# Performance work log

Hardware: AMD Instinct MI355X
Metric: run time of the kernel (lower is better)

Reference implementation:

```python
import jax, jax.numpy as jnp
import numpy as np

H = 16  # num_heads

def setup_inputs() -> dict:
    key = jax.random.key(0)
    ks = jax.random.split(key, 6)
    B, N, D = 2, 2048, 1024
    s = 0.02
    return {
        "x": jax.random.normal(ks[0], (B, N, D), jnp.float32),
        "attn_bias": jax.random.normal(ks[1], (B, N), jnp.float32),
        "w_qkv": jax.random.normal(ks[2], (D, 3 * D), jnp.float32) * s,
        "b_qkv": jnp.zeros((3 * D,), jnp.float32),
        "w_proj": jax.random.normal(ks[3], (D, D), jnp.float32) * s,
        "b_proj": jnp.zeros((D,), jnp.float32),
    }

def reference(x, attn_bias, w_qkv, b_qkv, w_proj, b_proj):
    B, N, D = x.shape
    hd = D // H
    qkv = x @ w_qkv + b_qkv                       # (B,N,3D)
    qkv = qkv.reshape(B, N, 3, H, hd)
    q, k, v = qkv[:, :, 0], qkv[:, :, 1], qkv[:, :, 2]  # (B,N,H,hd)
    scores = jnp.einsum("bqhd,bkhd->bhqk", q, k) / np.sqrt(hd).astype(x.dtype)
    scores = scores + attn_bias[:, None, None, :]  # key-wise bias (B,1,1,N)
    w = jax.nn.softmax(scores, axis=-1)
    out = jnp.einsum("bhqk,bkhd->bqhd", w, v).reshape(B, N, D)
    return out @ w_proj + b_proj
```

## Files before the change

kernel.cpp:

```cpp
#include <hip/hip_runtime.h>
#include <stdint.h>

typedef __attribute__((ext_vector_type(8))) short bf16x8;
typedef __attribute__((ext_vector_type(4))) short s16x4;
typedef __attribute__((ext_vector_type(4))) float f32x4;
typedef __attribute__((ext_vector_type(2))) unsigned int u32x2;
typedef __attribute__((ext_vector_type(4))) unsigned int u32x4;

#define DEV __device__ __forceinline__

DEV unsigned short f2bf(float f) {
    unsigned u = __builtin_bit_cast(unsigned, f);
    u += 0x7FFFu + ((u >> 16) & 1u);
    return (unsigned short)(u >> 16);
}

DEV void gload_lds16(const void* g, void* l) {
    __builtin_amdgcn_global_load_lds(
        (const __attribute__((address_space(1))) unsigned int*)g,
        (__attribute__((address_space(3))) unsigned int*)l,
        16, 0, 0);
}

__global__ __launch_bounds__(256) void cvt_f32_bf16(
    const float* __restrict__ in, unsigned short* __restrict__ out, int n4) {
    int i = blockIdx.x * blockDim.x + threadIdx.x;
    if (i >= n4) return;
    const float4 v = reinterpret_cast<const float4*>(in)[i];
    s16x4 o;
    o.x = (short)f2bf(v.x); o.y = (short)f2bf(v.y);
    o.z = (short)f2bf(v.z); o.w = (short)f2bf(v.w);
    reinterpret_cast<s16x4*>(out)[i] = o;
}

__global__ __launch_bounds__(256) void transpose_w(
    const float* __restrict__ w, unsigned short* __restrict__ wt, int K, int N) {
    __shared__ unsigned short tile[64][72];
    const int k0 = blockIdx.y * 64, n0 = blockIdx.x * 64;
    const int t = threadIdx.x;
    #pragma unroll
    for (int i = 0; i < 4; ++i) {
        const int e = t + i * 256;
        const int r = e >> 4, c4 = e & 15;
        const float4 v = *reinterpret_cast<const float4*>(w + (size_t)(k0 + r) * N + n0 + c4 * 4);
        s16x4 o;
        o.x = (short)f2bf(v.x); o.y = (short)f2bf(v.y);
        o.z = (short)f2bf(v.z); o.w = (short)f2bf(v.w);
        *(s16x4*)&tile[r][c4 * 4] = o;
    }
    __syncthreads();
    #pragma unroll
    for (int i = 0; i < 4; ++i) {
        const int e = t + i * 256;
        const int rn = e >> 4, c4 = e & 15;
        s16x4 o;
        o.x = (short)tile[c4 * 4 + 0][rn];
        o.y = (short)tile[c4 * 4 + 1][rn];
        o.z = (short)tile[c4 * 4 + 2][rn];
        o.w = (short)tile[c4 * 4 + 3][rn];
        *(s16x4*)(wt + (size_t)(n0 + rn) * K + k0 + c4 * 4) = o;
    }
}

__global__ __launch_bounds__(512, 2)
void gemm256_qkv(const unsigned short* __restrict__ A,
                 const unsigned short* __restrict__ BT,
                 const float* __restrict__ bias,
                 unsigned short* __restrict__ q_out,
                 unsigned short* __restrict__ k_out,
                 unsigned short* __restrict__ v_out)
{
    constexpr int K = 1024;
    constexpr int NT = 16;
    __shared__ unsigned short lds[2][2][2][2][128][32];

    const int t = threadIdx.x;
    const int wave = t >> 6, lane = t & 63;
    const int l15 = lane & 15, l4 = lane >> 4;
    const int wr = wave >> 2, wc = wave & 3;

    const int lin = blockIdx.x;
    const int logical = (lin & 7) * 24 + (lin >> 3);
    const int bx = logical % 12, by = logical / 12;
    const int tile_m = by * 256, tile_n = bx * 256;

    const int st_row = t >> 2;
    const int st_col = ((t & 3) ^ ((t >> 3) & 3)) * 8;
    const int cswz   = (l4 ^ ((l15 >> 1) & 3)) * 8;

    f32x4 acc[8][4] = {};
    bf16x8 ra[4], rb[4];

    #define STAGE(buf, ab, half, kk, k0)                                           \
        gload_lds16(((ab) ? BT : A) +                                              \
                        (size_t)(((ab) ? tile_n : tile_m) + (half) * 128 + st_row) * K \
                        + (k0) + (kk) * 32 + st_col,                               \
                    &lds[buf][ab][half][kk][0][0] + wave * 512)
    #define READ_A(buf, kk, mq)                                                    \
        _Pragma("unroll") for (int i = 0; i < 4; ++i)                              \
            ra[i] = *(const bf16x8*)&lds[buf][0][wr][kk][((mq) * 4 + i) * 16 + l15][cswz];
    #define READ_B(buf, kk)                                                        \
        _Pragma("unroll") for (int n = 0; n < 4; ++n)                              \
            rb[n] = *(const bf16x8*)&lds[buf][1][wc >> 1][kk][(wc & 1) * 64 + n * 16 + l15][cswz];
    #define MFMA16(mq)                                                             \
        __builtin_amdgcn_s_setprio(1);                                             \
        _Pragma("unroll") for (int i = 0; i < 4; ++i)                              \
            _Pragma("unroll") for (int n = 0; n < 4; ++n)                          \
                acc[(mq) * 4 + i][n] = __builtin_amdgcn_mfma_f32_16x16x32_bf16(    \
                    ra[i], rb[n], acc[(mq) * 4 + i][n], 0, 0, 0);                  \
        __builtin_amdgcn_s_setprio(0);
    #define BAR()   __builtin_amdgcn_s_barrier()
    #define LGKM0() do { asm volatile("s_waitcnt lgkmcnt(0)" ::: "memory");        \
                         __builtin_amdgcn_sched_barrier(0); } while (0)

    STAGE(0, 1, 0, 0, 0);  STAGE(0, 1, 1, 0, 0);
    STAGE(0, 0, 0, 0, 0);  STAGE(0, 0, 1, 0, 0);
    STAGE(0, 1, 0, 1, 0);  STAGE(0, 1, 1, 1, 0);
    STAGE(0, 0, 0, 1, 0);  STAGE(0, 0, 1, 1, 0);
    STAGE(1, 1, 0, 0, 64); STAGE(1, 1, 1, 0, 64);
    STAGE(1, 0, 0, 0, 64); STAGE(1, 0, 1, 0, 64);
    STAGE(1, 1, 0, 1, 64); STAGE(1, 1, 1, 1, 64);
    asm volatile("s_waitcnt vmcnt(6)" ::: "memory");
    BAR();

    for (int kt = 0; kt < NT; ++kt) {
        const int buf = kt & 1;
        const int k0 = kt * 64;
        const bool s1 = (kt + 1 < NT);
        const bool s234 = (kt + 2 < NT);

        READ_A(buf, 0, 0); READ_B(buf, 0);
        if (s1) { STAGE(buf ^ 1, 0, 0, 1, k0 + 64); STAGE(buf ^ 1, 0, 1, 1, k0 + 64); }
        BAR(); LGKM0();
        MFMA16(0);
        BAR();

        READ_A(buf, 0, 1);
        if (s234) { STAGE(buf, 1, 0, 0, k0 + 128); STAGE(buf, 1, 1, 0, k0 + 128); }
        BAR(); LGKM0();
        MFMA16(1);
        BAR();

        READ_A(buf, 1, 0); READ_B(buf, 1);
        if (s234) { STAGE(buf, 0, 0, 0, k0 + 128); STAGE(buf, 0, 1, 0, k0 + 128); }
        BAR(); LGKM0();
        MFMA16(0);
        BAR();

        READ_A(buf, 1, 1);
        if (s234) { STAGE(buf, 1, 0, 1, k0 + 128); STAGE(buf, 1, 1, 1, k0 + 128); }
        BAR(); LGKM0();
        MFMA16(1);
        if (kt < NT - 2)       asm volatile("s_waitcnt vmcnt(6)" ::: "memory");
        else if (kt == NT - 2) asm volatile("s_waitcnt vmcnt(0)" ::: "memory");
        if (kt < NT - 1) BAR();
    }
    #undef STAGE
    #undef READ_A
    #undef READ_B
    #undef MFMA16
    #undef BAR
    #undef LGKM0

    float bcol[4];
    #pragma unroll
    for (int n = 0; n < 4; ++n) bcol[n] = bias[tile_n + wc * 64 + n * 16 + l15];

    #pragma unroll
    for (int m = 0; m < 8; ++m)
        #pragma unroll
        for (int n = 0; n < 4; ++n) {
            const int col = tile_n + wc * 64 + n * 16 + l15;
            const int which = col >> 10;
            const int hh = (col >> 6) & 15;
            const int d = col & 63;
            #pragma unroll
            for (int r = 0; r < 4; ++r) {
                const int row = tile_m + wr * 128 + m * 16 + l4 * 4 + r;
                const float v = acc[m][n][r] + bcol[n];
                const int bb = row >> 11, nn = row & 2047;
                const size_t dst = ((size_t)((bb * 16 + hh) * 2048 + nn)) * 64 + d;
                if (which == 0)      q_out[dst] = f2bf(v * 0.18033688f);
                else if (which == 1) k_out[dst] = f2bf(v);
                else                 v_out[dst] = f2bf(v);
            }
        }
}

__global__ __launch_bounds__(256)
void gemm_bf16_f32out(const unsigned short* __restrict__ A,
                      const unsigned short* __restrict__ BT,
                      const float* __restrict__ bias,
                      float* __restrict__ f_out,
                      int M, int N, int K)
{
    __shared__ unsigned short Abuf[128 * 64];
    __shared__ unsigned short Bbuf[128 * 64];

    const int t = threadIdx.x;
    const int wave = t >> 6, lane = t & 63;
    const int l15 = lane & 15, l4 = lane >> 4;
    const int wr = wave >> 1, wc = wave & 1;
    const int tile_m = blockIdx.y * 128, tile_n = blockIdx.x * 128;

    const int srow = wave * 32 + (lane >> 3);
    const int scol = (lane & 7) * 8;

    f32x4 acc[4][4] = {};

    const int nk = K >> 6;
    for (int kt = 0; kt < nk; ++kt) {
        const int k0 = kt << 6;
        __syncthreads();
        #pragma unroll
        for (int c = 0; c < 4; ++c) {
            const unsigned short* sa = A + (size_t)(tile_m + srow + c * 8) * K + k0 + scol;
            gload_lds16(sa, &Abuf[(wave * 32 + c * 8) * 64]);
            const unsigned short* sb = BT + (size_t)(tile_n + srow + c * 8) * K + k0 + scol;
            gload_lds16(sb, &Bbuf[(wave * 32 + c * 8) * 64]);
        }
        asm volatile("s_waitcnt vmcnt(0)" ::: "memory");
        __syncthreads();

        bf16x8 ra[4][2], rb[4][2];
        #pragma unroll
        for (int m = 0; m < 4; ++m)
            #pragma unroll
            for (int ks = 0; ks < 2; ++ks)
                ra[m][ks] = *(const bf16x8*)&Abuf[(wr * 64 + m * 16 + l15) * 64 + ks * 32 + l4 * 8];
        #pragma unroll
        for (int n = 0; n < 4; ++n)
            #pragma unroll
            for (int ks = 0; ks < 2; ++ks)
                rb[n][ks] = *(const bf16x8*)&Bbuf[(wc * 64 + n * 16 + l15) * 64 + ks * 32 + l4 * 8];

        #pragma unroll
        for (int m = 0; m < 4; ++m)
            #pragma unroll
            for (int n = 0; n < 4; ++n) {
                acc[m][n] = __builtin_amdgcn_mfma_f32_16x16x32_bf16(ra[m][0], rb[n][0], acc[m][n], 0, 0, 0);
                acc[m][n] = __builtin_amdgcn_mfma_f32_16x16x32_bf16(ra[m][1], rb[n][1], acc[m][n], 0, 0, 0);
            }
    }

    float bcol[4];
    #pragma unroll
    for (int n = 0; n < 4; ++n) bcol[n] = bias[tile_n + wc * 64 + n * 16 + l15];

    #pragma unroll
    for (int m = 0; m < 4; ++m)
        #pragma unroll
        for (int n = 0; n < 4; ++n) {
            const int col = tile_n + wc * 64 + n * 16 + l15;
            #pragma unroll
            for (int r = 0; r < 4; ++r) {
                const int row = tile_m + wr * 64 + m * 16 + l4 * 4 + r;
                f_out[(size_t)row * N + col] = acc[m][n][r] + bcol[n];
            }
        }
}

__global__ __launch_bounds__(512, 4)
void attn_kernel(const unsigned short* __restrict__ Qb,
                 const unsigned short* __restrict__ Kb,
                 const unsigned short* __restrict__ Vb,
                 const float* __restrict__ bias,
                 unsigned short* __restrict__ Ob)
{
    __shared__ __align__(16) unsigned char pool[45056];
    unsigned short (*Klds)[64][72] = (unsigned short (*)[64][72])(pool);
    unsigned short (*Vlds)[64][72] = (unsigned short (*)[64][72])(pool + 18432);
    float* blds = (float*)(pool + 36864);
    float (*Oscr)[32][64] = (float (*)[32][64])(pool);
    float (*Lscr)[4][32]  = (float (*)[4][32])(pool + 32768);

    const unsigned di = blockIdx.x;
    const unsigned logical = (di & 7) * 64 + (di >> 3);
    const int qt = logical & 15;
    const int h  = (logical >> 4) & 15;
    const int b  = logical >> 8;

    const int t = threadIdx.x;
    const int wave = t >> 6, lane = t & 63;
    const int l15 = lane & 15, l4 = lane >> 4;
    const int wq = wave & 3, wk = wave >> 2;
    const int kb0 = wk * 32;

    const size_t head = ((size_t)(b * 16 + h)) * 2048 * 64;
    const unsigned short* Qh = Qb + head;
    const unsigned short* Kh = Kb + head;
    const unsigned short* Vh = Vb + head;

    for (int i = t; i < 2048; i += 512) blds[i] = bias[b * 2048 + i] * 1.44269504f - 8.0f;

    const int qbase = qt * 128 + wq * 32;
    bf16x8 qf[2][2];
    #pragma unroll
    for (int qi = 0; qi < 2; ++qi)
        #pragma unroll
        for (int ks = 0; ks < 2; ++ks)
            qf[qi][ks] = *(const bf16x8*)(Qh + (size_t)(qbase + qi * 16 + l15) * 64 + ks * 32 + l4 * 8);

    float lsum[2] = {0.f, 0.f};
    f32x4 oacc[2][4] = {};

    const int ts = t & 255;
    const int kr = ts >> 3, kc = (ts & 7) * 8;
    const int vkp = (ts & 31) * 2;
    const int vd0 = (ts >> 5) * 8;
    const int vsp = (vkp & 32) | (((vkp >> 2) & 3) << 3) | (((vkp >> 4) & 1) << 2) | (vkp & 3);

    bf16x8 st0, st1;
    if (wk == 0) {
        st0 = *(const bf16x8*)(Kh + (size_t)(kr) * 64 + kc);
        st1 = *(const bf16x8*)(Kh + (size_t)(32 + kr) * 64 + kc);
    } else {
        st0 = *(const bf16x8*)(Vh + (size_t)(vkp) * 64 + vd0);
        st1 = *(const bf16x8*)(Vh + (size_t)(vkp + 1) * 64 + vd0);
    }

    for (int kt = 0; kt < 32; ++kt) {
        const int key0 = kt * 64;
        const int pb = kt & 1;

        if (wk == 0) {
            *(bf16x8*)&Klds[pb][kr][kc] = st0;
            *(bf16x8*)&Klds[pb][32 + kr][kc] = st1;
        } else {
            #pragma unroll
            for (int j = 0; j < 8; ++j) {
                unsigned pr = (unsigned)(unsigned short)st0[j] | ((unsigned)(unsigned short)st1[j] << 16);
                *(unsigned*)&Vlds[pb][vd0 + j][vsp] = pr;
            }
        }

        if (kt < 31) {
            const int nk0 = key0 + 64;
            if (wk == 0) {
                st0 = *(const bf16x8*)(Kh + (size_t)(nk0 + kr) * 64 + kc);
                st1 = *(const bf16x8*)(Kh + (size_t)(nk0 + 32 + kr) * 64 + kc);
            } else {
                st0 = *(const bf16x8*)(Vh + (size_t)(nk0 + vkp) * 64 + vd0);
                st1 = *(const bf16x8*)(Vh + (size_t)(nk0 + vkp + 1) * 64 + vd0);
            }
        }

        __syncthreads();

        bf16x8 kfr[2][2];
        #pragma unroll
        for (int f = 0; f < 2; ++f)
            #pragma unroll
            for (int ks = 0; ks < 2; ++ks)
                kfr[f][ks] = *(const bf16x8*)&Klds[pb][kb0 + f * 16 + l15][ks * 32 + l4 * 8];

        f32x4 bk[2];
        #pragma unroll
        for (int f = 0; f < 2; ++f)
            bk[f] = *(const f32x4*)&blds[key0 + kb0 + f * 16 + l4 * 4];

        f32x4 s[2][2];
        __builtin_amdgcn_s_setprio(1);
        #pragma unroll
        for (int qi = 0; qi < 2; ++qi)
            #pragma unroll
            for (int f = 0; f < 2; ++f) {
                f32x4 z = bk[f];
                z = __builtin_amdgcn_mfma_f32_16x16x32_bf16(kfr[f][0], qf[qi][0], z, 0, 0, 0);
                z = __builtin_amdgcn_mfma_f32_16x16x32_bf16(kfr[f][1], qf[qi][1], z, 0, 0, 0);
                s[qi][f] = z;
            }
        __builtin_amdgcn_s_setprio(0);

        bf16x8 pa[2];
        #pragma unroll
        for (int qi = 0; qi < 2; ++qi) {
            float ps = 0.f;
            u32x4 w;
            #pragma unroll
            for (int f = 0; f < 2; ++f) {
                const float p0 = exp2f(s[qi][f][0]);
                const float p1 = exp2f(s[qi][f][1]);
                const float p2 = exp2f(s[qi][f][2]);
                const float p3 = exp2f(s[qi][f][3]);
                ps += (p0 + p1) + (p2 + p3);
                unsigned w0, w1;
                asm("v_cvt_pk_bf16_f32 %0, %1, %2" : "=v"(w0) : "v"(p0), "v"(p1));
                asm("v_cvt_pk_bf16_f32 %0, %1, %2" : "=v"(w1) : "v"(p2), "v"(p3));
                w[f * 2] = w0; w[f * 2 + 1] = w1;
            }
            lsum[qi] += ps;
            pa[qi] = __builtin_bit_cast(bf16x8, w);
        }

        __builtin_amdgcn_s_setprio(1);
        #pragma unroll
        for (int df = 0; df < 4; ++df) {
            bf16x8 vf = *(const bf16x8*)&Vlds[pb][df * 16 + l15][kb0 + l4 * 8];
            oacc[0][df] = __builtin_amdgcn_mfma_f32_16x16x32_bf16(pa[0], vf, oacc[0][df], 0, 0, 0);
            oacc[1][df] = __builtin_amdgcn_mfma_f32_16x16x32_bf16(pa[1], vf, oacc[1][df], 0, 0, 0);
        }
        __builtin_amdgcn_s_setprio(0);
    }

    #pragma unroll
    for (int qi = 0; qi < 2; ++qi) {
        lsum[qi] += __shfl_xor(lsum[qi], 16, 64);
        lsum[qi] += __shfl_xor(lsum[qi], 32, 64);
    }

    __syncthreads();
    if (lane < 16) {
        Lscr[wk][wq][lane] = lsum[0];
        Lscr[wk][wq][16 + lane] = lsum[1];
    }
    if (wk == 1) {
        #pragma unroll
        for (int qi = 0; qi < 2; ++qi)
            #pragma unroll
            for (int df = 0; df < 4; ++df)
                #pragma unroll
                for (int r = 0; r < 4; ++r)
                    Oscr[wq][qi * 16 + l4 * 4 + r][df * 16 + l15] = oacc[qi][df][r];
    }
    __syncthreads();
    if (wk == 0) {
        #pragma unroll
        for (int qi = 0; qi < 2; ++qi) {
            float inv[4];
            #pragma unroll
            for (int r = 0; r < 4; ++r) {
                const int ql = qi * 16 + l4 * 4 + r;
                inv[r] = 1.0f / (Lscr[0][wq][ql] + Lscr[1][wq][ql]);
            }
            #pragma unroll
            for (int r = 0; r < 4; ++r) {
                const int ql = qi * 16 + l4 * 4 + r;
                const int q = qbase + ql;
                #pragma unroll
                for (int df = 0; df < 4; ++df) {
                    const int d = df * 16 + l15;
                    const float v = oacc[qi][df][r] + Oscr[wq][ql][d];
                    Ob[((size_t)(b * 2048 + q)) * 1024 + h * 64 + d] = f2bf(v * inv[r]);
                }
            }
        }
    }
}

extern "C" void kernel_launch(void* const* d_in, const int* in_sizes, int n_in,
                              void* d_out, int out_size, void* d_ws, size_t ws_size,
                              hipStream_t stream) {
    const float* x      = (const float*)d_in[0];
    const float* abias  = (const float*)d_in[1];
    const float* w_qkv  = (const float*)d_in[2];
    const float* b_qkv  = (const float*)d_in[3];
    const float* w_proj = (const float*)d_in[4];
    const float* b_proj = (const float*)d_in[5];
    float* out = (float*)d_out;

    unsigned short* ws = (unsigned short*)d_ws;
    unsigned short* xb  = ws;
    unsigned short* wqT = xb  + (size_t)4096 * 1024;
    unsigned short* wpT = wqT + (size_t)3072 * 1024;
    unsigned short* qb  = wpT + (size_t)1024 * 1024;
    unsigned short* kb  = qb  + (size_t)2 * 16 * 2048 * 64;
    unsigned short* vb  = kb  + (size_t)2 * 16 * 2048 * 64;
    unsigned short* ao  = vb  + (size_t)2 * 16 * 2048 * 64;

    cvt_f32_bf16<<<4096, 256, 0, stream>>>(x, xb, 1048576);
    transpose_w<<<dim3(48, 16), 256, 0, stream>>>(w_qkv, wqT, 1024, 3072);
    transpose_w<<<dim3(16, 16), 256, 0, stream>>>(w_proj, wpT, 1024, 1024);
    gemm256_qkv<<<192, 512, 0, stream>>>(xb, wqT, b_qkv, qb, kb, vb);
    attn_kernel<<<512, 512, 0, stream>>>(qb, kb, vb, abias, ao);
    gemm_bf16_f32out<<<dim3(8, 32), 256, 0, stream>>>(ao, wpT, b_proj, out, 4096, 1024, 1024);
}
```

Measured before the change: 131.4 us.

## Store V pre-transposed from QKV GEMM and stream K/V via direct global-to-LDS loads

The QKV GEMM epilogue now writes V in a transposed, key-permuted layout, packing four values per store. The attention kernel then loads K and V tiles with global_load_lds straight into XOR-swizzled unpadded LDS buffers, replacing register staging and the per-element V transpose. This is meant to cut VGPR pressure, LDS write instructions and bank conflicts in the attention inner loop. In exchange, the V stores in the GEMM epilogue become more scattered and the sync point moves to the end of each iteration.

```diff
diff --git a/kernel.cpp b/kernel.cpp
--- a/kernel.cpp
+++ b/kernel.cpp
@@ -4,7 +4,6 @@
 typedef __attribute__((ext_vector_type(8))) short bf16x8;
 typedef __attribute__((ext_vector_type(4))) short s16x4;
 typedef __attribute__((ext_vector_type(4))) float f32x4;
-typedef __attribute__((ext_vector_type(2))) unsigned int u32x2;
 typedef __attribute__((ext_vector_type(4))) unsigned int u32x4;
 
 #define DEV __device__ __forceinline__
@@ -174,15 +173,24 @@
             const int which = col >> 10;
             const int hh = (col >> 6) & 15;
             const int d = col & 63;
-            #pragma unroll
-            for (int r = 0; r < 4; ++r) {
-                const int row = tile_m + wr * 128 + m * 16 + l4 * 4 + r;
-                const float v = acc[m][n][r] + bcol[n];
-                const int bb = row >> 11, nn = row & 2047;
-                const size_t dst = ((size_t)((bb * 16 + hh) * 2048 + nn)) * 64 + d;
-                if (which == 0)      q_out[dst] = f2bf(v * 0.18033688f);
-                else if (which == 1) k_out[dst] = f2bf(v);
-                else                 v_out[dst] = f2bf(v);
+            const int row0 = tile_m + wr * 128 + m * 16 + l4 * 4;
+            const int bb = row0 >> 11, nn = row0 & 2047;
+            if (which == 2) {
+                const int nl = nn & 63;
+                const int np = (nl & 32) | ((nl & 12) << 1) | ((nl & 16) >> 2) | (nl & 3);
+                const size_t dstV = ((size_t)((bb * 16 + hh) * 64 + d)) * 2048 + (nn & ~63) + np;
+                s16x4 pk;
+                #pragma unroll
+                for (int r = 0; r < 4; ++r) pk[r] = (short)f2bf(acc[m][n][r] + bcol[n]);
+                *(s16x4*)&v_out[dstV] = pk;
+            } else {
+                #pragma unroll
+                for (int r = 0; r < 4; ++r) {
+                    const float v = acc[m][n][r] + bcol[n];
+                    const size_t dst = ((size_t)((bb * 16 + hh) * 2048 + nn + r)) * 64 + d;
+                    if (which == 0) q_out[dst] = f2bf(v * 0.18033688f);
+                    else            k_out[dst] = f2bf(v);
+                }
             }
         }
 }
@@ -263,14 +271,14 @@
 __global__ __launch_bounds__(512, 4)
 void attn_kernel(const unsigned short* __restrict__ Qb,
                  const unsigned short* __restrict__ Kb,
-                 const unsigned short* __restrict__ Vb,
+                 const unsigned short* __restrict__ Vt,
                  const float* __restrict__ bias,
                  unsigned short* __restrict__ Ob)
 {
-    __shared__ __align__(16) unsigned char pool[45056];
-    unsigned short (*Klds)[64][72] = (unsigned short (*)[64][72])(pool);
-    unsigned short (*Vlds)[64][72] = (unsigned short (*)[64][72])(pool + 18432);
-    float* blds = (float*)(pool + 36864);
+    __shared__ __align__(16) unsigned char pool[40960];
+    unsigned short (*Kf)[4096] = (unsigned short (*)[4096])(pool);
+    unsigned short (*Vf)[4096] = (unsigned short (*)[4096])(pool + 16384);
+    float* blds = (float*)(pool + 32768);
     float (*Oscr)[32][64] = (float (*)[32][64])(pool);
     float (*Lscr)[4][32]  = (float (*)[4][32])(pool + 32768);
 
@@ -285,11 +293,16 @@
     const int l15 = lane & 15, l4 = lane >> 4;
     const int wq = wave & 3, wk = wave >> 2;
     const int kb0 = wk * 32;
+    const int xsw = (l15 & 7) << 3;
 
     const size_t head = ((size_t)(b * 16 + h)) * 2048 * 64;
     const unsigned short* Qh = Qb + head;
     const unsigned short* Kh = Kb + head;
-    const unsigned short* Vh = Vb + head;
+
+    const int srow8 = wave * 8 + (lane >> 3);
+    const int scol8 = 8 * ((lane & 7) ^ (lane >> 3));
+    const unsigned short* Ksrc = Kh + (size_t)srow8 * 64 + scol8;
+    const unsigned short* Vsrc = Vt + ((size_t)((b * 16 + h) * 64) + srow8) * 2048 + scol8;
 
     for (int i = t; i < 2048; i += 512) blds[i] = bias[b * 2048 + i] * 1.44269504f - 8.0f;
 
@@ -304,55 +317,28 @@
     float lsum[2] = {0.f, 0.f};
     f32x4 oacc[2][4] = {};
 
-    const int ts = t & 255;
-    const int kr = ts >> 3, kc = (ts & 7) * 8;
-    const int vkp = (ts & 31) * 2;
-    const int vd0 = (ts >> 5) * 8;
-    const int vsp = (vkp & 32) | (((vkp >> 2) & 3) << 3) | (((vkp >> 4) & 1) << 2) | (vkp & 3);
-
-    bf16x8 st0, st1;
-    if (wk == 0) {
-        st0 = *(const bf16x8*)(Kh + (size_t)(kr) * 64 + kc);
-        st1 = *(const bf16x8*)(Kh + (size_t)(32 + kr) * 64 + kc);
-    } else {
-        st0 = *(const bf16x8*)(Vh + (size_t)(vkp) * 64 + vd0);
-        st1 = *(const bf16x8*)(Vh + (size_t)(vkp + 1) * 64 + vd0);
-    }
+    gload_lds16(Ksrc, &Kf[0][wave * 512]);
+    gload_lds16(Vsrc, &Vf[0][wave * 512]);
+    __syncthreads();
 
     for (int kt = 0; kt < 32; ++kt) {
         const int key0 = kt * 64;
         const int pb = kt & 1;
 
-        if (wk == 0) {
-            *(bf16x8*)&Klds[pb][kr][kc] = st0;
-            *(bf16x8*)&Klds[pb][32 + kr][kc] = st1;
-        } else {
-            #pragma unroll
-            for (int j = 0; j < 8; ++j) {
-                unsigned pr = (unsigned)(unsigned short)st0[j] | ((unsigned)(unsigned short)st1[j] << 16);
-                *(unsigned*)&Vlds[pb][vd0 + j][vsp] = pr;
-            }
-        }
-
         if (kt < 31) {
-            const int nk0 = key0 + 64;
-            if (wk == 0) {
-                st0 = *(const bf16x8*)(Kh + (size_t)(nk0 + kr) * 64 + kc);
-                st1 = *(const bf16x8*)(Kh + (size_t)(nk0 + 32 + kr) * 64 + kc);
-            } else {
-                st0 = *(const bf16x8*)(Vh + (size_t)(nk0 + vkp) * 64 + vd0);
-                st1 = *(const bf16x8*)(Vh + (size_t)(nk0 + vkp + 1) * 64 + vd0);
-            }
-        }
-
-        __syncthreads();
+            gload_lds16(Ksrc + (size_t)(key0 + 64) * 64, &Kf[pb ^ 1][wave * 512]);
+            gload_lds16(Vsrc + key0 + 64, &Vf[pb ^ 1][wave * 512]);
+        }
+
+        const unsigned short* Kp = Kf[pb];
+        const unsigned short* Vp = Vf[pb];
 
         bf16x8 kfr[2][2];
         #pragma unroll
         for (int f = 0; f < 2; ++f)
             #pragma unroll
             for (int ks = 0; ks < 2; ++ks)
-                kfr[f][ks] = *(const bf16x8*)&Klds[pb][kb0 + f * 16 + l15][ks * 32 + l4 * 8];
+                kfr[f][ks] = *(const bf16x8*)&Kp[(kb0 + f * 16 + l15) * 64 + ((ks * 32 + l4 * 8) ^ xsw)];
 
         f32x4 bk[2];
         #pragma unroll
@@ -396,11 +382,13 @@
         __builtin_amdgcn_s_setprio(1);
         #pragma unroll
         for (int df = 0; df < 4; ++df) {
-            bf16x8 vf = *(const bf16x8*)&Vlds[pb][df * 16 + l15][kb0 + l4 * 8];
+            bf16x8 vf = *(const bf16x8*)&Vp[(df * 16 + l15) * 64 + ((kb0 + l4 * 8) ^ xsw)];
             oacc[0][df] = __builtin_amdgcn_mfma_f32_16x16x32_bf16(pa[0], vf, oacc[0][df], 0, 0, 0);
             oacc[1][df] = __builtin_amdgcn_mfma_f32_16x16x32_bf16(pa[1], vf, oacc[1][df], 0, 0, 0);
         }
         __builtin_amdgcn_s_setprio(0);
+
+        __syncthreads();
     }
 
     #pragma unroll
@@ -465,13 +453,13 @@
     unsigned short* wpT = wqT + (size_t)3072 * 1024;
     unsigned short* qb  = wpT + (size_t)1024 * 1024;
     unsigned short* kb  = qb  + (size_t)2 * 16 * 2048 * 64;
-    unsigned short* vb  = kb  + (size_t)2 * 16 * 2048 * 64;
-    unsigned short* ao  = vb  + (size_t)2 * 16 * 2048 * 64;
+    unsigned short* vt  = kb  + (size_t)2 * 16 * 2048 * 64;
+    unsigned short* ao  = vt  + (size_t)2 * 16 * 2048 * 64;
 
     cvt_f32_bf16<<<4096, 256, 0, stream>>>(x, xb, 1048576);
     transpose_w<<<dim3(48, 16), 256, 0, stream>>>(w_qkv, wqT, 1024, 3072);
     transpose_w<<<dim3(16, 16), 256, 0, stream>>>(w_proj, wpT, 1024, 1024);
-    gemm256_qkv<<<192, 512, 0, stream>>>(xb, wqT, b_qkv, qb, kb, vb);
-    attn_kernel<<<512, 512, 0, stream>>>(qb, kb, vb, abias, ao);
+    gemm256_qkv<<<192, 512, 0, stream>>>(xb, wqT, b_qkv, qb, kb, vt);
+    attn_kernel<<<512, 512, 0, stream>>>(qb, kb, vt, abias, ao);
     gemm_bf16_f32out<<<dim3(8, 32), 256, 0, stream>>>(ao, wpT, b_proj, out, 4096, 1024, 1024);
 }
```

Measured after the change: 130.2 us. About the same (-0.9%).
